# Kernel optimization log

Measured on AMD Instinct MI355X. Metric: run time of the kernel, lower is better.

Reference implementation:

```python
import jax, jax.numpy as jnp
import numpy as np

B, D, T = 16, 256, 2048
K = 8192
COMMITMENT_COST = 0.25


def setup_inputs() -> dict:
    key = jax.random.key(0)
    k1, k2 = jax.random.split(key)
    z = jax.random.normal(k1, (B, D, T), dtype=jnp.float32)
    # original init: uniform(-1/K, 1/K)
    emb = jax.random.uniform(k2, (K, D), dtype=jnp.float32, minval=-1.0 / K, maxval=1.0 / K)
    return {"z": z, "emb": emb}


def reference(z, emb):
    b, d, t = z.shape
    zf = z.transpose(0, 2, 1).reshape(-1, d)  # [N, D], N = b*t
    # squared euclidean distances [N, K]
    distances = (
        jnp.sum(zf * zf, axis=1, keepdims=True)
        + jnp.sum(emb * emb, axis=1)
        - 2.0 * zf @ emb.T
    )
    idx = jnp.argmin(distances, axis=1)  # [N]
    # direct gather instead of one-hot matmul (same math)
    quantized = emb[idx].reshape(b, t, d).transpose(0, 2, 1)  # [B, D, T]
    e_latent_loss = jnp.mean((jax.lax.stop_gradient(quantized) - z) ** 2)
    q_latent_loss = jnp.mean((quantized - jax.lax.stop_gradient(z)) ** 2)
    loss = q_latent_loss + COMMITMENT_COST * e_latent_loss
    quantized_st = z + jax.lax.stop_gradient(quantized - z)  # straight-through
    return quantized_st, loss, idx[:, None]
```

## Files before the change

### kernel.cpp

```cpp
#include <hip/hip_runtime.h>
#include <cstdint>

#define BB 16
#define DD 256
#define TT 2048
#define KK 8192
#define NN 32768
#define QQ 8388608
typedef unsigned long long u64;

typedef __attribute__((ext_vector_type(8))) short short8;
typedef __attribute__((ext_vector_type(4))) float f32x4;

#define GLOBAL_AS __attribute__((address_space(1)))
#define LDS_AS    __attribute__((address_space(3)))

__device__ __forceinline__ void async_copy16(void* l, const void* g) {
    __builtin_amdgcn_global_load_lds((const GLOBAL_AS unsigned int*)g,
                                     (LDS_AS unsigned int*)l, 16, 0, 0);
}

__device__ __forceinline__ unsigned mapf(float f) {
    unsigned u = __float_as_uint(f);
    return (u & 0x80000000u) ? ~u : (u | 0x80000000u);
}
__device__ __forceinline__ float unmapf(unsigned u) {
    return __uint_as_float((u & 0x80000000u) ? (u & 0x7FFFFFFFu) : ~u);
}
__device__ __forceinline__ unsigned bf16_rne(float v) {
    unsigned ui = __float_as_uint(v);
    return (ui + 0x7FFFu + ((ui >> 16) & 1)) >> 16;
}

__global__ __launch_bounds__(256) void k_prepA(const float* __restrict__ z,
                                               float* __restrict__ A32,
                                               int* __restrict__ cnt,
                                               float* __restrict__ out) {
    __shared__ double sd[256];
    int tid = threadIdx.x;
    int r = tid & 63;
    int c = tid >> 6;
    int n = blockIdx.x * 64 + r;
    if (blockIdx.x == 0 && tid == 0) { *cnt = 0; out[QQ] = 0.0f; }
    int b = n >> 11, t = n & 2047;
    const float* zp = z + (size_t)b * 524288 + t;
    double s = 0.0;
#pragma unroll 8
    for (int i = 0; i < 64; i++) {
        float v = zp[(size_t)(c * 64 + i) * 2048];
        s = fma((double)v, (double)v, s);
    }
    sd[tid] = s;
    __syncthreads();
    if (c == 0) {
        double tot = sd[r] + sd[64 + r] + sd[128 + r] + sd[192 + r];
        A32[n] = (float)tot;
    }
}

__global__ __launch_bounds__(256) void k_convZ(const float* __restrict__ z,
                                               unsigned short* __restrict__ zh,
                                               unsigned short* __restrict__ zl) {
    __shared__ float sm[64][65];
    int tid = threadIdx.x;
    int bid = blockIdx.x;
    int b  = bid >> 7;
    int dt = (bid >> 5) & 3;
    int tt = bid & 31;
    const float* zp = z + (size_t)b * 524288 + (size_t)dt * 131072 + tt * 64;
#pragma unroll
    for (int i = 0; i < 16; i++) {
        int idx = tid + 256 * i;
        int d = idx >> 6, t = idx & 63;
        sm[d][t] = zp[(size_t)d * 2048 + t];
    }
    __syncthreads();
    int d0 = (tid & 7) * 8;
#pragma unroll
    for (int i = 0; i < 2; i++) {
        int t = (tid >> 3) + 32 * i;
        size_t o = ((size_t)(b * 2048 + tt * 64 + t)) * 256 + dt * 64 + d0;
        short8 hv, lv;
#pragma unroll
        for (int j = 0; j < 8; j++) {
            float v = sm[d0 + j][t];
            unsigned hb = bf16_rne(v);
            float hf = __uint_as_float(hb << 16);
            unsigned lb = bf16_rne(v - hf);
            hv[j] = (short)hb;
            lv[j] = (short)lb;
        }
        *(short8*)(zh + o) = hv;
        *(short8*)(zl + o) = lv;
    }
}

__global__ __launch_bounds__(256) void k_convE(const float* __restrict__ emb,
                                               unsigned short* __restrict__ eh,
                                               unsigned short* __restrict__ el) {
    int base = (blockIdx.x * 256 + threadIdx.x) * 8;
    float4 v0 = *(const float4*)(emb + base);
    float4 v1 = *(const float4*)(emb + base + 4);
    float vv[8] = {v0.x, v0.y, v0.z, v0.w, v1.x, v1.y, v1.z, v1.w};
    short8 hv, lv;
#pragma unroll
    for (int i = 0; i < 8; i++) {
        unsigned hb = bf16_rne(vv[i]);
        float hf = __uint_as_float(hb << 16);
        unsigned lb = bf16_rne(vv[i] - hf);
        hv[i] = (short)hb;
        lv[i] = (short)lb;
    }
    *(short8*)(eh + base) = hv;
    *(short8*)(el + base) = lv;
}

__global__ __launch_bounds__(512, 2) void k_gemm(const unsigned short* __restrict__ zh,
                                                 const unsigned short* __restrict__ zl,
                                                 const unsigned short* __restrict__ eh,
                                                 const unsigned short* __restrict__ el,
                                                 u64* __restrict__ cand) {
    __shared__ __align__(16) unsigned short pool[2][32768];

    int tid  = threadIdx.x;
    int w    = __builtin_amdgcn_readfirstlane(tid >> 6);
    int lane = tid & 63;
    int lm   = lane & 15;
    int q    = lane >> 4;
    int wm   = w >> 1;
    int wn   = w & 1;

    int bid = blockIdx.x;
    int tl  = (bid & 7) * 128 + (bid >> 3);
    int mt  = tl >> 3;
    int ng  = tl & 7;

    int laneoff = lm * 256 + q * 8;
    const unsigned short* gp[8];
    unsigned dlo[8];
    bool bflag[8];
#pragma unroll
    for (int i = 0; i < 8; i++) {
        int slot = w * 8 + i;
        int arr  = slot >> 4;
        int tile = slot & 15;
        const unsigned short* s = (arr == 0) ? zh : (arr == 1) ? zl
                                : (arr == 2) ? eh : el;
        int rowb = (arr < 2) ? mt * 256 : ng * 1024;
        gp[i]    = s + (size_t)(rowb + tile * 16) * 256 + laneoff;
        dlo[i]   = (unsigned)(arr * 8192 + tile * 512);
        bflag[i] = (arr >= 2);
    }

    float v1a[4][4], v2a[4][4];
    int   i1a[4][4];
#pragma unroll
    for (int mi = 0; mi < 4; mi++)
#pragma unroll
        for (int reg = 0; reg < 4; reg++) {
            v1a[mi][reg] = -3.4e38f; v2a[mi][reg] = -3.4e38f;
            i1a[mi][reg] = 0;
        }

    f32x4 acc[4][8];

#pragma unroll
    for (int i = 0; i < 8; i++)
        async_copy16(&pool[0][dlo[i]], gp[i]);

    for (int t = 0; t < 32; ++t) {
        int buf = t & 1;
        int kc  = t & 7;

        asm volatile("s_waitcnt vmcnt(0)" ::: "memory");
        __builtin_amdgcn_s_barrier();
        __builtin_amdgcn_sched_barrier(0);

        int tn = t + 1;
        if (tn < 32) {
            if ((tn & 7) == 0) {
#pragma unroll
                for (int i = 0; i < 8; i++)
                    if (bflag[i]) gp[i] += 65536;
            }
            int nkc = tn & 7;
#pragma unroll
            for (int i = 0; i < 8; i++)
                async_copy16(&pool[buf ^ 1][dlo[i]], gp[i] + nkc * 32);
        }

        if (kc == 0) {
#pragma unroll
            for (int mi = 0; mi < 4; mi++)
#pragma unroll
                for (int ni = 0; ni < 8; ni++) acc[mi][ni] = (f32x4){0.f, 0.f, 0.f, 0.f};
        }

        const unsigned short* pb = pool[buf];
        short8 azh[4], azl[4];
#pragma unroll
        for (int mi = 0; mi < 4; mi++) {
            azh[mi] = *(const short8*)&pb[(wm * 4 + mi) * 512 + lane * 8];
            azl[mi] = *(const short8*)&pb[8192 + (wm * 4 + mi) * 512 + lane * 8];
        }
        __builtin_amdgcn_s_setprio(1);
#pragma unroll
        for (int ni = 0; ni < 8; ni++) {
            short8 bh = *(const short8*)&pb[16384 + (wn * 8 + ni) * 512 + lane * 8];
            short8 bl = *(const short8*)&pb[24576 + (wn * 8 + ni) * 512 + lane * 8];
#pragma unroll
            for (int mi = 0; mi < 4; mi++) {
                acc[mi][ni] = __builtin_amdgcn_mfma_f32_16x16x32_bf16(azh[mi], bh, acc[mi][ni], 0, 0, 0);
                acc[mi][ni] = __builtin_amdgcn_mfma_f32_16x16x32_bf16(azl[mi], bh, acc[mi][ni], 0, 0, 0);
                acc[mi][ni] = __builtin_amdgcn_mfma_f32_16x16x32_bf16(azh[mi], bl, acc[mi][ni], 0, 0, 0);
            }
        }
        __builtin_amdgcn_s_setprio(0);

        if (kc == 7) {
            int idb = ng * 1024 + (t >> 3) * 256 + wn * 128 + lm;
#pragma unroll
            for (int ni = 0; ni < 8; ni++) {
                int id = idb + ni * 16;
#pragma unroll
                for (int mi = 0; mi < 4; mi++)
#pragma unroll
                    for (int reg = 0; reg < 4; reg++) {
                        float v = acc[mi][ni][reg];
                        bool c1 = v > v1a[mi][reg];
                        bool c2 = v > v2a[mi][reg];
                        v2a[mi][reg] = c2 ? v : v2a[mi][reg];
                        v2a[mi][reg] = c1 ? v1a[mi][reg] : v2a[mi][reg];
                        v1a[mi][reg] = c1 ? v : v1a[mi][reg];
                        i1a[mi][reg] = c1 ? id : i1a[mi][reg];
                    }
            }
        }
    }

    u64* rtop = (u64*)&pool[0][0];
#pragma unroll
    for (int mi = 0; mi < 4; mi++)
#pragma unroll
        for (int reg = 0; reg < 4; reg++) {
            u64 p1 = ((u64)mapf(-2.0f * v1a[mi][reg]) << 32) | (unsigned)i1a[mi][reg];
            u64 p2 = ((u64)mapf(-2.0f * v2a[mi][reg]) << 32);
#pragma unroll
            for (int msk = 1; msk <= 8; msk <<= 1) {
                u64 q1 = __shfl_xor(p1, msk, 64);
                u64 q2 = __shfl_xor(p2, msk, 64);
                u64 n1 = (p1 < q1) ? p1 : q1;
                u64 hi = (p1 < q1) ? q1 : p1;
                u64 n2 = (q2 < p2) ? q2 : p2;
                n2 = (hi < n2) ? hi : n2;
                p1 = n1; p2 = n2;
            }
            if (lm == 0) {
                int rl = wm * 64 + mi * 16 + q * 4 + reg;
                rtop[rl * 4 + wn * 2]     = p1;
                rtop[rl * 4 + wn * 2 + 1] = p2;
            }
        }
    __syncthreads();
    if (tid < 256) {
        u64 a1 = rtop[tid * 4],     a2 = rtop[tid * 4 + 1];
        u64 b1 = rtop[tid * 4 + 2], b2 = rtop[tid * 4 + 3];
        u64 m1 = (a1 < b1) ? a1 : b1;
        u64 lo = (a1 < b1) ? b1 : a1;
        u64 m2 = (a2 < b2) ? a2 : b2;
        m2 = (lo < m2) ? lo : m2;
        size_t o = ((size_t)ng * 32768 + (size_t)mt * 256 + tid) * 2;
        cand[o]     = m1;
        cand[o + 1] = m2;
    }
}

__global__ __launch_bounds__(256) void k_select(const u64* __restrict__ cand,
                                                const float* __restrict__ A32,
                                                int* __restrict__ keys,
                                                int* __restrict__ cnt,
                                                int* __restrict__ list) {
    int n = blockIdx.x * 256 + threadIdx.x;
    u64 m1 = cand[(size_t)n * 2];
    u64 m2 = cand[(size_t)n * 2 + 1];
#pragma unroll
    for (int j = 1; j < 8; j++) {
        u64 c1 = cand[((size_t)j * 32768 + n) * 2];
        u64 c2 = cand[((size_t)j * 32768 + n) * 2 + 1];
        if (c1 < m1) { m2 = (m1 < m2) ? m1 : m2; m1 = c1; }
        else         { m2 = (c1 < m2) ? c1 : m2; }
        m2 = (c2 < m2) ? c2 : m2;
    }
    keys[n] = (int)(unsigned)(m1 & 0xFFFFFFFFull);
    float f1 = unmapf((unsigned)(m1 >> 32));
    float f2 = unmapf((unsigned)(m2 >> 32));
    float W = ((A32[n] >= 255.9f) ? 3.4e-5f : 1.8e-5f) + 4e-6f;
    if (f2 - f1 <= W) {
        int p = atomicAdd(cnt, 1);
        list[p] = n;
    }
}

__global__ __launch_bounds__(256) void k_argmin_fb(const float* __restrict__ z,
                                                   const float* __restrict__ emb,
                                                   u64* __restrict__ cand2) {
    __shared__ __align__(16) float smem[8192];
    float* As = smem;
    float* Bs = smem + 4096;

    int tid = threadIdx.x;
    int tx  = tid & 15;
    int ty  = tid >> 4;
    int mt  = blockIdx.x;
    int kh  = blockIdx.y;

    int bimg = mt >> 4;
    int t0   = (mt & 15) << 7;
    const float* zb = z + (size_t)bimg * (DD * TT) + t0;

    float bestv[8], bestv2[8];
    int   besti[8];
#pragma unroll
    for (int i = 0; i < 8; i++) { bestv[i] = 3.4e38f; bestv2[i] = 3.4e38f; besti[i] = 0; }

    int qa = tid & 31, ra = tid >> 5;
    int jb = tid >> 3, db = tid & 7;
    int swz_t = (tx & 7) << 2;

    for (int kc = 0; kc < 32; kc++) {
        int k0 = kh * 4096 + kc * 128;
        float acc[8][8];
#pragma unroll
        for (int i = 0; i < 8; i++)
#pragma unroll
            for (int j = 0; j < 8; j++) acc[i][j] = 0.0f;

        for (int dc = 0; dc < 8; dc++) {
            int d0 = dc * 32;
            __syncthreads();
#pragma unroll
            for (int s = 0; s < 4; s++) {
                int d = ra + 8 * s;
                float4 v = *(const float4*)(zb + (size_t)(d0 + d) * TT + 4 * qa);
                *(float4*)(As + d * 128 + 4 * qa) = v;
            }
#pragma unroll
            for (int s = 0; s < 4; s++) {
                int row = jb + 32 * s;
                float4 v = *(const float4*)(emb + (size_t)(k0 + row) * DD + d0 + 4 * db);
                int col  = (4 * db) ^ ((row & 7) << 2);
                *(float4*)(Bs + row * 32 + col) = v;
            }
            __syncthreads();
#pragma unroll
            for (int g = 0; g < 8; g++) {
                float4 bf[8];
#pragma unroll
                for (int in = 0; in < 8; in++) {
                    int nn = in * 16 + tx;
                    bf[in] = *(const float4*)(Bs + nn * 32 + ((4 * g) ^ swz_t));
                }
#pragma unroll
                for (int j = 0; j < 4; j++) {
                    int d = 4 * g + j;
                    float4 a0 = *(const float4*)(As + d * 128 + ty * 8);
                    float4 a1 = *(const float4*)(As + d * 128 + ty * 8 + 4);
                    float av[8] = {a0.x, a0.y, a0.z, a0.w, a1.x, a1.y, a1.z, a1.w};
#pragma unroll
                    for (int im = 0; im < 8; im++) {
#pragma unroll
                        for (int in = 0; in < 8; in++) {
                            const float* bfp = (const float*)&bf[in];
                            acc[im][in] = fmaf(av[im], bfp[j], acc[im][in]);
                        }
                    }
                }
            }
        }
#pragma unroll
        for (int in = 0; in < 8; in++) {
            int k = k0 + in * 16 + tx;
#pragma unroll
            for (int im = 0; im < 8; im++) {
                float s = -2.0f * acc[im][in];
                if (s < bestv[im]) { bestv2[im] = bestv[im]; bestv[im] = s; besti[im] = k; }
                else if (s < bestv2[im]) { bestv2[im] = s; }
            }
        }
    }

    __syncthreads();
    u64* red = (u64*)smem;
#pragma unroll
    for (int im = 0; im < 8; im++) {
        int r = ty * 8 + im;
        red[r * 32 + tx * 2 + 0] = ((u64)mapf(bestv[im]) << 32) | (unsigned)besti[im];
        red[r * 32 + tx * 2 + 1] = ((u64)mapf(bestv2[im]) << 32);
    }
    __syncthreads();
    if (tid < 128) {
        const u64* base = red + tid * 32;
        u64 p1 = base[0];
        u64 s2 = base[1];
#pragma unroll
        for (int t = 1; t < 16; t++) {
            u64 c1 = base[t * 2], c2 = base[t * 2 + 1];
            if (c1 < p1) { s2 = (p1 < s2) ? p1 : s2; p1 = c1; }
            else         { s2 = (c1 < s2) ? c1 : s2; }
            s2 = (c2 < s2) ? c2 : s2;
        }
        int n = mt * 128 + tid;
        cand2[(size_t)n * 4 + kh * 2]     = p1;
        cand2[(size_t)n * 4 + kh * 2 + 1] = s2;
    }
}

__global__ __launch_bounds__(256) void k_select_fb(const u64* __restrict__ cand2,
                                                   const float* __restrict__ A32,
                                                   int* __restrict__ keys,
                                                   int* __restrict__ cnt,
                                                   int* __restrict__ list) {
    int n = blockIdx.x * 256 + threadIdx.x;
    u64 a1 = cand2[(size_t)n * 4 + 0], a2 = cand2[(size_t)n * 4 + 1];
    u64 b1 = cand2[(size_t)n * 4 + 2], b2 = cand2[(size_t)n * 4 + 3];
    u64 m1 = (a1 < b1) ? a1 : b1;
    u64 lo = (a1 < b1) ? b1 : a1;
    u64 m2 = (a2 < b2) ? a2 : b2;
    m2 = (lo < m2) ? lo : m2;

    keys[n] = (int)(unsigned)(m1 & 0xFFFFFFFFull);
    float f1 = unmapf((unsigned)(m1 >> 32));
    float f2 = unmapf((unsigned)(m2 >> 32));
    float W = (A32[n] >= 255.9f) ? 3.4e-5f : 1.8e-5f;
    if (f2 - f1 <= W) {
        int p = atomicAdd(cnt, 1);
        list[p] = n;
    }
}

__global__ __launch_bounds__(256) void k_refine(const float* __restrict__ z,
                                                const float* __restrict__ emb,
                                                const float* __restrict__ A32,
                                                const int* __restrict__ list,
                                                const int* __restrict__ cnt,
                                                int* __restrict__ keys) {
    __shared__ __align__(16) float zs[256][8];
    __shared__ float aA[8];
    __shared__ int   ln[8];
    __shared__ u64   wred[4 * 8];

    int tid = threadIdx.x, lane = tid & 63, w = tid >> 6;
    int count = *cnt;
    int ngroups = (count + 7) >> 3;

    for (int g = blockIdx.x; g < ngroups; g += gridDim.x) {
        __syncthreads();
#pragma unroll
        for (int r = 0; r < 8; r++) {
            int row = g * 8 + r;
            int n   = list[(row < count) ? row : 0];
            int b = n >> 11, t = n & 2047;
            zs[tid][r] = z[(size_t)b * (DD * TT) + (size_t)tid * TT + t];
            if (tid == 0) { ln[r] = (row < count) ? n : -1; aA[r] = A32[n]; }
        }
        __syncthreads();

        u64 best[8];
#pragma unroll
        for (int r = 0; r < 8; r++) best[r] = 0xFFFFFFFFFFFFFFFFull;

        float Ar[8];
#pragma unroll
        for (int r = 0; r < 8; r++) Ar[r] = aA[r];

        for (int c = 0; c < 8; c++) {
            int kbase = c * 1024 + tid;
            const float4* e0 = (const float4*)(emb + (size_t)(kbase)       * DD);
            const float4* e1 = (const float4*)(emb + (size_t)(kbase + 256) * DD);
            const float4* e2 = (const float4*)(emb + (size_t)(kbase + 512) * DD);
            const float4* e3 = (const float4*)(emb + (size_t)(kbase + 768) * DD);
            float acc[4][8];
#pragma unroll
            for (int qq = 0; qq < 4; qq++)
#pragma unroll
                for (int r = 0; r < 8; r++) acc[qq][r] = 0.0f;

            for (int d4 = 0; d4 < 64; d4++) {
                float4 v0 = e0[d4], v1 = e1[d4], v2 = e2[d4], v3 = e3[d4];
                const float* p0 = (const float*)&v0;
                const float* p1 = (const float*)&v1;
                const float* p2 = (const float*)&v2;
                const float* p3 = (const float*)&v3;
#pragma unroll
                for (int i = 0; i < 4; i++) {
                    int d = 4 * d4 + i;
                    float4 za = *(const float4*)&zs[d][0];
                    float4 zb2 = *(const float4*)&zs[d][4];
                    const float* zr  = (const float*)&za;
                    const float* zr2 = (const float*)&zb2;
#pragma unroll
                    for (int r = 0; r < 4; r++) {
                        acc[0][r]     = fmaf(zr[r],  p0[i], acc[0][r]);
                        acc[1][r]     = fmaf(zr[r],  p1[i], acc[1][r]);
                        acc[2][r]     = fmaf(zr[r],  p2[i], acc[2][r]);
                        acc[3][r]     = fmaf(zr[r],  p3[i], acc[3][r]);
                        acc[0][r + 4] = fmaf(zr2[r], p0[i], acc[0][r + 4]);
                        acc[1][r + 4] = fmaf(zr2[r], p1[i], acc[1][r + 4]);
                        acc[2][r + 4] = fmaf(zr2[r], p2[i], acc[2][r + 4]);
                        acc[3][r + 4] = fmaf(zr2[r], p3[i], acc[3][r + 4]);
                    }
                }
            }
#pragma unroll
            for (int qq = 0; qq < 4; qq++) {
                int k = kbase + qq * 256;
#pragma unroll
                for (int r = 0; r < 8; r++) {
                    float dk = Ar[r] - 2.0f * acc[qq][r];
                    u64 p = ((u64)mapf(dk) << 32) | (unsigned)k;
                    best[r] = (p < best[r]) ? p : best[r];
                }
            }
        }
#pragma unroll
        for (int r = 0; r < 8; r++) {
            u64 v = best[r];
            for (int off = 32; off; off >>= 1) {
                u64 o = __shfl_down(v, off, 64);
                v = (o < v) ? o : v;
            }
            if (lane == 0) wred[w * 8 + r] = v;
        }
        __syncthreads();
        if (tid < 8) {
            u64 v = wred[tid];
#pragma unroll
            for (int j = 1; j < 4; j++) {
                u64 o = wred[j * 8 + tid];
                v = (o < v) ? o : v;
            }
            int n = ln[tid];
            if (n >= 0) keys[n] = (int)(unsigned)(v & 0xFFFFFFFFull);
        }
        __syncthreads();
    }
}

__global__ __launch_bounds__(256) void k_out(const float* __restrict__ z,
                                             const float* __restrict__ emb,
                                             const int* __restrict__ keys,
                                             float* __restrict__ out) {
    int tid = threadIdx.x;
    int n   = blockIdx.x * 256 + tid;
    int b   = n >> 11;
    int t   = n & 2047;
    int idx = keys[n];
    out[QQ + 1 + n] = (float)idx;

    const float4* erow = (const float4*)(emb + (size_t)idx * DD);
    const float*  zp   = z   + (size_t)b * (DD * TT) + t;
    float*        op   = out + (size_t)b * (DD * TT) + t;

    float ssd = 0.0f;
#pragma unroll 4
    for (int d4 = 0; d4 < 64; d4++) {
        float4 qv = erow[d4];
        float qa[4] = {qv.x, qv.y, qv.z, qv.w};
#pragma unroll
        for (int r = 0; r < 4; r++) {
            int d = 4 * d4 + r;
            float zv = zp[(size_t)d * TT];
            float df = qa[r] - zv;
            ssd = fmaf(df, df, ssd);
            op[(size_t)d * TT] = qa[r];
        }
    }
    for (int off = 32; off; off >>= 1) ssd += __shfl_down(ssd, off, 64);
    __shared__ float red[4];
    if ((tid & 63) == 0) red[tid >> 6] = ssd;
    __syncthreads();
    if (tid == 0) {
        float tot = red[0] + red[1] + red[2] + red[3];
        atomicAdd(out + QQ, tot * (1.25f / (float)QQ));
    }
}

extern "C" void kernel_launch(void* const* d_in, const int* in_sizes, int n_in,
                              void* d_out, int out_size, void* d_ws, size_t ws_size,
                              hipStream_t stream) {
    const float* z   = (const float*)d_in[0];
    const float* emb = (const float*)d_in[1];
    float* out = (float*)d_out;

    char* ws = (char*)d_ws;
    const size_t oZH = 0;
    const size_t oZL = oZH + 16777216;
    const size_t oEH = oZL + 16777216;
    const size_t oEL = oEH + 4194304;
    const size_t oCD = oEL + 4194304;
    const size_t oA3 = oCD + 4194304;
    const size_t oKY = oA3 + 131072;
    const size_t oLS = oKY + 131072;
    const size_t oCN = oLS + 131072;
    const size_t needed = oCN + 64;

    if (ws_size >= needed) {
        unsigned short* zh = (unsigned short*)(ws + oZH);
        unsigned short* zl = (unsigned short*)(ws + oZL);
        unsigned short* eh = (unsigned short*)(ws + oEH);
        unsigned short* el = (unsigned short*)(ws + oEL);
        u64*   cand = (u64*)(ws + oCD);
        float* A32  = (float*)(ws + oA3);
        int*   keys = (int*)(ws + oKY);
        int*   list = (int*)(ws + oLS);
        int*   cnt  = (int*)(ws + oCN);

        k_prepA <<<512,  256, 0, stream>>>(z, A32, cnt, out);
        k_convZ <<<2048, 256, 0, stream>>>(z, zh, zl);
        k_convE <<<1024, 256, 0, stream>>>(emb, eh, el);
        k_gemm  <<<1024, 512, 0, stream>>>(zh, zl, eh, el, cand);
        k_select<<<128,  256, 0, stream>>>(cand, A32, keys, cnt, list);
        k_refine<<<512,  256, 0, stream>>>(z, emb, A32, list, cnt, keys);
        k_out   <<<128,  256, 0, stream>>>(z, emb, keys, out);
    } else {
        u64*   cand2 = (u64*)ws;
        float* A32   = (float*)(ws + 1048576);
        int*   keys  = (int*)(ws + 1048576 + 131072);
        int*   list  = (int*)(ws + 1048576 + 262144);
        int*   cnt   = (int*)(ws + 1048576 + 393216);

        k_prepA    <<<512,          256, 0, stream>>>(z, A32, cnt, out);
        k_argmin_fb<<<dim3(256, 2), 256, 0, stream>>>(z, emb, cand2);
        k_select_fb<<<128,          256, 0, stream>>>(cand2, A32, keys, cnt, list);
        k_refine   <<<512,          256, 0, stream>>>(z, emb, A32, list, cnt, keys);
        k_out      <<<128,          256, 0, stream>>>(z, emb, keys, out);
    }
}
```

Baseline: 950.5 us.

## Track second-best indices and rescore top candidates exactly in select kernel

The GEMM epilogue now records the index of the second-best candidate as well, so each row carries 16 candidate indices across the 8 codebook groups. The select kernel recomputes exact fp32 distances for these 16 candidates per row and takes the best, which lets it skip the full refine pass for rows where the only near-tie is within the top candidates. Only rows whose eighth-group second-best is within the tolerance window still go to the refine list. This adds strided per-thread z and emb loads in select (256 dims times 16 gathers) and extra register pressure in the GEMM epilogue, traded against fewer rows sent to k_refine.

```diff
diff --git a/kernel.cpp b/kernel.cpp
--- a/kernel.cpp
+++ b/kernel.cpp
@@ -153,13 +153,13 @@
     }
 
     float v1a[4][4], v2a[4][4];
-    int   i1a[4][4];
+    int   i1a[4][4], i2a[4][4];
 #pragma unroll
     for (int mi = 0; mi < 4; mi++)
 #pragma unroll
         for (int reg = 0; reg < 4; reg++) {
             v1a[mi][reg] = -3.4e38f; v2a[mi][reg] = -3.4e38f;
-            i1a[mi][reg] = 0;
+            i1a[mi][reg] = 0;        i2a[mi][reg] = 0;
         }
 
     f32x4 acc[4][8];
@@ -227,11 +227,13 @@
 #pragma unroll
                     for (int reg = 0; reg < 4; reg++) {
                         float v = acc[mi][ni][reg];
+                        bool c2 = v > v2a[mi][reg];
                         bool c1 = v > v1a[mi][reg];
-                        bool c2 = v > v2a[mi][reg];
-                        v2a[mi][reg] = c2 ? v : v2a[mi][reg];
+                        v2a[mi][reg] = c2 ? v  : v2a[mi][reg];
+                        i2a[mi][reg] = c2 ? id : i2a[mi][reg];
                         v2a[mi][reg] = c1 ? v1a[mi][reg] : v2a[mi][reg];
-                        v1a[mi][reg] = c1 ? v : v1a[mi][reg];
+                        i2a[mi][reg] = c1 ? i1a[mi][reg] : i2a[mi][reg];
+                        v1a[mi][reg] = c1 ? v  : v1a[mi][reg];
                         i1a[mi][reg] = c1 ? id : i1a[mi][reg];
                     }
             }
@@ -244,7 +246,7 @@
 #pragma unroll
         for (int reg = 0; reg < 4; reg++) {
             u64 p1 = ((u64)mapf(-2.0f * v1a[mi][reg]) << 32) | (unsigned)i1a[mi][reg];
-            u64 p2 = ((u64)mapf(-2.0f * v2a[mi][reg]) << 32);
+            u64 p2 = ((u64)mapf(-2.0f * v2a[mi][reg]) << 32) | (unsigned)i2a[mi][reg];
 #pragma unroll
             for (int msk = 1; msk <= 8; msk <<= 1) {
                 u64 q1 = __shfl_xor(p1, msk, 64);
@@ -276,29 +278,63 @@
 }
 
 __global__ __launch_bounds__(256) void k_select(const u64* __restrict__ cand,
+                                                const float* __restrict__ z,
+                                                const float* __restrict__ emb,
                                                 const float* __restrict__ A32,
                                                 int* __restrict__ keys,
                                                 int* __restrict__ cnt,
                                                 int* __restrict__ list) {
     int n = blockIdx.x * 256 + threadIdx.x;
-    u64 m1 = cand[(size_t)n * 2];
-    u64 m2 = cand[(size_t)n * 2 + 1];
-#pragma unroll
-    for (int j = 1; j < 8; j++) {
-        u64 c1 = cand[((size_t)j * 32768 + n) * 2];
-        u64 c2 = cand[((size_t)j * 32768 + n) * 2 + 1];
-        if (c1 < m1) { m2 = (m1 < m2) ? m1 : m2; m1 = c1; }
-        else         { m2 = (c1 < m2) ? c1 : m2; }
-        m2 = (c2 < m2) ? c2 : m2;
-    }
-    keys[n] = (int)(unsigned)(m1 & 0xFFFFFFFFull);
-    float f1 = unmapf((unsigned)(m1 >> 32));
-    float f2 = unmapf((unsigned)(m2 >> 32));
-    float W = ((A32[n] >= 255.9f) ? 3.4e-5f : 1.8e-5f) + 4e-6f;
-    if (f2 - f1 <= W) {
+    u64 p1[8], p2[8];
+    u64 m1 = ~0ull;
+#pragma unroll
+    for (int j = 0; j < 8; j++) {
+        p1[j] = cand[((size_t)j * 32768 + n) * 2];
+        p2[j] = cand[((size_t)j * 32768 + n) * 2 + 1];
+        m1 = (p1[j] < m1) ? p1[j] : m1;
+    }
+    float f1   = unmapf((unsigned)(m1 >> 32));
+    float A32v = A32[n];
+    float W = ((A32v >= 255.9f) ? 3.4e-5f : 1.8e-5f) + 4e-6f;
+
+    bool flag = false;
+#pragma unroll
+    for (int j = 0; j < 8; j++)
+        flag |= (unmapf((unsigned)(p2[j] >> 32)) - f1 <= W);
+
+    if (flag) {
+        keys[n] = (int)(unsigned)(m1 & 0xFFFFFFFFull);
         int p = atomicAdd(cnt, 1);
         list[p] = n;
-    }
+        return;
+    }
+
+    int idx[16];
+#pragma unroll
+    for (int j = 0; j < 8; j++) {
+        idx[2 * j]     = (int)(unsigned)(p1[j] & 0xFFFFFFFFull);
+        idx[2 * j + 1] = (int)(unsigned)(p2[j] & 0xFFFFFFFFull);
+    }
+    float acc[16];
+#pragma unroll
+    for (int c = 0; c < 16; c++) acc[c] = 0.0f;
+
+    int b = n >> 11, t = n & 2047;
+    const float* zp = z + (size_t)b * 524288 + t;
+    for (int d = 0; d < 256; d++) {
+        float zv = zp[(size_t)d * 2048];
+#pragma unroll
+        for (int c = 0; c < 16; c++)
+            acc[c] = fmaf(zv, emb[(size_t)idx[c] * 256 + d], acc[c]);
+    }
+    u64 best = ~0ull;
+#pragma unroll
+    for (int c = 0; c < 16; c++) {
+        float dk = A32v - 2.0f * acc[c];
+        u64 p = ((u64)mapf(dk) << 32) | (unsigned)idx[c];
+        best = (p < best) ? p : best;
+    }
+    keys[n] = (int)(unsigned)(best & 0xFFFFFFFFull);
 }
 
 __global__ __launch_bounds__(256) void k_argmin_fb(const float* __restrict__ z,
@@ -619,7 +655,7 @@
         k_convZ <<<2048, 256, 0, stream>>>(z, zh, zl);
         k_convE <<<1024, 256, 0, stream>>>(emb, eh, el);
         k_gemm  <<<1024, 512, 0, stream>>>(zh, zl, eh, el, cand);
-        k_select<<<128,  256, 0, stream>>>(cand, A32, keys, cnt, list);
+        k_select<<<128,  256, 0, stream>>>(cand, z, emb, A32, keys, cnt, list);
         k_refine<<<512,  256, 0, stream>>>(z, emb, A32, list, cnt, keys);
         k_out   <<<128,  256, 0, stream>>>(z, emb, keys, out);
     } else {
```

Measured after the change: 1.125 ms. 18.4% more time.
